# Performance work log

Measured on AMD Instinct MI355X. Metric: run time of the kernel, lower is better.

Reference implementation:

```python
import jax, jax.numpy as jnp
import numpy as np

P = 512        # n_predicates
C = 65536      # n_constants
L = 1          # max_rule_length (only runnable config of original code)


def setup_inputs() -> dict:
    key = jax.random.key(0)
    k1, k2 = jax.random.split(key)
    initial_facts = jax.random.uniform(k1, (P, C), dtype=jnp.float32)
    rule_weights = jax.random.normal(k2, (P, L, P), dtype=jnp.float32)
    return {"initial_facts": initial_facts, "rule_weights": rule_weights, "n_iterations": 3}


def reference(initial_facts, rule_weights, n_iterations):
    # F.softmax(rule[step], dim=0) on the 1-D vector rule_weights[r, 0, :]
    # == softmax over the last axis of rule_weights[:, 0, :].
    # Stacking apply_rule over all rules r is exactly A @ facts.
    A = jax.nn.softmax(rule_weights[:, 0, :], axis=-1)  # [P, P]
    facts = initial_facts                                # [P, C]
    for _ in range(n_iterations):
        derived = A @ facts                              # [P, C] (rule r -> row r)
        facts = jnp.maximum(facts, derived.max(axis=0))  # broadcast [C] over [P, C]
    return facts
```

## Files before the change

### kernel.cpp

```cpp
#include <hip/hip_runtime.h>
#include <hip/hip_bf16.h>
#include <cstdint>


typedef __attribute__((ext_vector_type(8))) short bf16x8;
typedef __attribute__((ext_vector_type(8))) unsigned short u16x8;
typedef __attribute__((ext_vector_type(4))) float f32x4;
typedef unsigned short ushort_t;
typedef unsigned int uint32;

#define PDIM 512
#define CDIM 65536
#define NT   64

__device__ __forceinline__ ushort_t f2bf(float x) {
    uint32 u = __float_as_uint(x);
    return (ushort_t)((u + 0x7fffu + ((u >> 16) & 1u)) >> 16);
}
__device__ __forceinline__ float bf2f(uint32 bits) { return __uint_as_float(bits << 16); }

__device__ __forceinline__ bf16x8 pkmax8(bf16x8 v, ushort_t mu) {
    u16x8 a = __builtin_bit_cast(u16x8, v);
    const u16x8 mb = {mu, mu, mu, mu, mu, mu, mu, mu};
    a = __builtin_elementwise_max(a, mb);
    return __builtin_bit_cast(bf16x8, a);
}

__global__ __launch_bounds__(64) void softmax_pack(const float* __restrict__ rw,
                                                   ushort_t* __restrict__ Apk) {
    const int r  = blockIdx.x;
    const int ln = threadIdx.x;
    const float* row = rw + r * PDIM;
    float4 x0 = *(const float4*)(row + ln * 8);
    float4 x1 = *(const float4*)(row + ln * 8 + 4);
    float v[8] = {x0.x, x0.y, x0.z, x0.w, x1.x, x1.y, x1.z, x1.w};

    float mx = -1e30f;
    #pragma unroll
    for (int i = 0; i < 8; ++i) mx = fmaxf(mx, v[i]);
    #pragma unroll
    for (int d = 1; d < 64; d <<= 1) mx = fmaxf(mx, __shfl_xor(mx, d, 64));
    float s = 0.f;
    #pragma unroll
    for (int i = 0; i < 8; ++i) { v[i] = __expf(v[i] - mx); s += v[i]; }
    #pragma unroll
    for (int d = 1; d < 64; d <<= 1) s += __shfl_xor(s, d, 64);
    const float inv = 1.f / s;

    ushort_t o[8];
    #pragma unroll
    for (int i = 0; i < 8; ++i) o[i] = f2bf(v[i] * inv);
    const int idx16 = (ln >> 2) * 2048 + (r >> 4) * 64 + ((ln & 3) << 4) + (r & 15);
    *(int4*)(Apk + idx16 * 8) = *(const int4*)o;
}

__global__ __launch_bounds__(256, 2) void ilp_kernel(
        const float* __restrict__ facts,
        const ushort_t* __restrict__ Apk,
        const int* __restrict__ n_iter_p,
        float* __restrict__ out) {
    __shared__ ushort_t ft[NT * PDIM];
    __shared__ float wred[2][4][NT];
    __shared__ float mfin[NT];

    const int tid  = threadIdx.x;
    const int wave = tid >> 6;
    const int lane = tid & 63;
    const int l15  = lane & 15;
    const int quad = lane >> 4;
    const int c0   = blockIdx.x * NT;

    {
        const int ch = (tid & 31) * 2;
        const int pb = tid >> 5;
        #pragma unroll 4
        for (int s = 0; s < 8; ++s) {
            const int p0 = s * 64 + pb * 8;
            ushort_t ga[8], gb[8];
            #pragma unroll
            for (int i = 0; i < 8; ++i) {
                const float2 v = *(const float2*)(facts + (p0 + i) * CDIM + c0 + ch);
                ga[i] = f2bf(v.x);
                gb[i] = f2bf(v.y);
            }
            const int g = p0 >> 3;
            *(int4*)(&ft[ch * PDIM + ((g ^ (ch & 7)) << 3)])             = *(const int4*)ga;
            *(int4*)(&ft[(ch + 1) * PDIM + ((g ^ ((ch + 1) & 7)) << 3)]) = *(const int4*)gb;
        }
    }
    __syncthreads();

    int n_iter = *n_iter_p;
    n_iter = n_iter < 0 ? 0 : (n_iter > 8 ? 8 : n_iter);

    const int abase = wave * 4096 + lane * 8;
    int cbase[4], cx8[4];
    #pragma unroll
    for (int ct = 0; ct < 4; ++ct) {
        const int c = ct * 16 + l15;
        cbase[ct] = c * PDIM;
        cx8[ct]   = (c & 7) * 8;
    }

    ushort_t ml[4] = {0, 0, 0, 0};
    float    mf[4] = {0.f, 0.f, 0.f, 0.f};

    bf16x8 aF[2][8], bF[2][4];
    {
        const ushort_t* ap = Apk + abase;
        #pragma unroll
        for (int rt = 0; rt < 8; ++rt) aF[0][rt] = *(const bf16x8*)(ap + rt * 512);
    }

    #pragma unroll 1
    for (int it = 0; it < n_iter; ++it) {
        f32x4 acc[8][4];
        #pragma unroll
        for (int rt = 0; rt < 8; ++rt)
            #pragma unroll
            for (int ct = 0; ct < 4; ++ct) acc[rt][ct] = (f32x4){0.f, 0.f, 0.f, 0.f};

        {
            const int g8 = quad * 8;
            #pragma unroll
            for (int ct = 0; ct < 4; ++ct)
                bF[0][ct] = pkmax8(*(const bf16x8*)(&ft[cbase[ct] + (g8 ^ cx8[ct])]), ml[ct]);
        }

        #pragma unroll 2
        for (int kt = 0; kt < 16; ++kt) {
            const int cur = kt & 1, nxt = cur ^ 1;
            const int ktn = (kt + 1) & 15;
            {
                const ushort_t* ap = Apk + abase + ktn * 16384;
                #pragma unroll
                for (int rt = 0; rt < 8; ++rt) aF[nxt][rt] = *(const bf16x8*)(ap + rt * 512);
            }
            {
                const int g8 = (ktn * 4 + quad) * 8;
                #pragma unroll
                for (int ct = 0; ct < 4; ++ct)
                    bF[nxt][ct] = pkmax8(*(const bf16x8*)(&ft[cbase[ct] + (g8 ^ cx8[ct])]), ml[ct]);
            }
            __builtin_amdgcn_s_setprio(1);
            #pragma unroll
            for (int rt = 0; rt < 8; ++rt)
                #pragma unroll
                for (int ct = 0; ct < 4; ++ct)
                    acc[rt][ct] = __builtin_amdgcn_mfma_f32_16x16x32_bf16(
                        aF[cur][rt], bF[cur][ct], acc[rt][ct], 0, 0, 0);
            __builtin_amdgcn_s_setprio(0);
        }

        float mx[4];
        #pragma unroll
        for (int ct = 0; ct < 4; ++ct) {
            float m0 = -1e30f;
            #pragma unroll
            for (int rt = 0; rt < 8; ++rt)
                #pragma unroll
                for (int e = 0; e < 4; ++e) m0 = fmaxf(m0, acc[rt][ct][e]);
            m0 = fmaxf(m0, __shfl_xor(m0, 16, 64));
            m0 = fmaxf(m0, __shfl_xor(m0, 32, 64));
            mx[ct] = m0;
        }
        const int buf = it & 1;
        if (quad == 0) {
            #pragma unroll
            for (int ct = 0; ct < 4; ++ct) wred[buf][wave][ct * 16 + l15] = mx[ct];
        }
        __syncthreads();
        #pragma unroll
        for (int ct = 0; ct < 4; ++ct) {
            const int c = ct * 16 + l15;
            const float m = fmaxf(fmaxf(wred[buf][0][c], wred[buf][1][c]),
                                  fmaxf(wred[buf][2][c], wred[buf][3][c]));
            mf[ct] = fmaxf(mf[ct], m);
            ml[ct] = f2bf(mf[ct]);
        }
    }

    if (wave == 0 && quad == 0) {
        #pragma unroll
        for (int ct = 0; ct < 4; ++ct) mfin[ct * 16 + l15] = mf[ct];
    }
    __syncthreads();

    {
        const int ch = (tid & 31) * 2;
        const int pb = tid >> 5;
        const float ma = mfin[ch];
        const float mb = mfin[ch + 1];
        for (int s = 0; s < 8; ++s) {
            const int p0 = s * 64 + pb * 8;
            const int g = p0 >> 3;
            ushort_t ga[8], gb[8];
            *(int4*)ga = *(const int4*)(&ft[ch * PDIM + ((g ^ (ch & 7)) << 3)]);
            *(int4*)gb = *(const int4*)(&ft[(ch + 1) * PDIM + ((g ^ ((ch + 1) & 7)) << 3)]);
            #pragma unroll
            for (int i = 0; i < 8; ++i) {
                float2 v;
                v.x = fmaxf(bf2f(ga[i]), ma);
                v.y = fmaxf(bf2f(gb[i]), mb);
                *(float2*)(out + (p0 + i) * CDIM + c0 + ch) = v;
            }
        }
    }
}

extern "C" void kernel_launch(void* const* d_in, const int* in_sizes, int n_in,
                              void* d_out, int out_size, void* d_ws, size_t ws_size,
                              hipStream_t stream) {
    const float* facts    = (const float*)d_in[0];
    const float* rw       = (const float*)d_in[1];
    const int*   n_iter_p = (const int*)d_in[2];
    float* out = (float*)d_out;

    ushort_t* Apk = (ushort_t*)d_ws;

    softmax_pack<<<PDIM, 64, 0, stream>>>(rw, Apk);
    ilp_kernel<<<CDIM / NT, 256, 0, stream>>>(facts, Apk, n_iter_p, out);
}
```

Measured before the change: 302.6 us.

## Switch matmul to 32x32x16 bf16 MFMA with repacked A and new LDS swizzle

Replaces the 16x16x32 MFMA tiling with 32x32x16 MFMA tiles. The softmax pack kernel's A layout and the LDS swizzle key for the facts tile are changed to match the new operand layout. The pkmax of the B operand is now applied after the prefetch rather than at load time, and the column-max reduction needs one fewer cross-lane shuffle. The aim is fewer MFMA issues and operand loads per K step. The larger per-instruction latency changes how the loop pipelines, and the LDS bank-conflict behaviour of the new swizzle is not certain.

```diff
diff --git a/kernel.cpp b/kernel.cpp
--- a/kernel.cpp
+++ b/kernel.cpp
@@ -5,7 +5,7 @@
 
 typedef __attribute__((ext_vector_type(8))) short bf16x8;
 typedef __attribute__((ext_vector_type(8))) unsigned short u16x8;
-typedef __attribute__((ext_vector_type(4))) float f32x4;
+typedef __attribute__((ext_vector_type(16))) float f32x16;
 typedef unsigned short ushort_t;
 typedef unsigned int uint32;
 
@@ -50,7 +50,7 @@
     ushort_t o[8];
     #pragma unroll
     for (int i = 0; i < 8; ++i) o[i] = f2bf(v[i] * inv);
-    const int idx16 = (ln >> 2) * 2048 + (r >> 4) * 64 + ((ln & 3) << 4) + (r & 15);
+    const int idx16 = ((ln >> 1) * 16 + (r >> 5)) * 64 + ((ln & 1) << 5) + (r & 31);
     *(int4*)(Apk + idx16 * 8) = *(const int4*)o;
 }
 
@@ -66,13 +66,17 @@
     const int tid  = threadIdx.x;
     const int wave = tid >> 6;
     const int lane = tid & 63;
-    const int l15  = lane & 15;
-    const int quad = lane >> 4;
+    const int l31  = lane & 31;
+    const int half = lane >> 5;
     const int c0   = blockIdx.x * NT;
 
+    int n_iter = *n_iter_p;
+    n_iter = n_iter < 0 ? 0 : (n_iter > 8 ? 8 : n_iter);
+
     {
-        const int ch = (tid & 31) * 2;
-        const int pb = tid >> 5;
+        const int ch  = (tid & 31) * 2;
+        const int pb  = tid >> 5;
+        const int key = ((ch >> 1) & 7) << 3;
         #pragma unroll 4
         for (int s = 0; s < 8; ++s) {
             const int p0 = s * 64 + pb * 8;
@@ -83,120 +87,118 @@
                 ga[i] = f2bf(v.x);
                 gb[i] = f2bf(v.y);
             }
-            const int g = p0 >> 3;
-            *(int4*)(&ft[ch * PDIM + ((g ^ (ch & 7)) << 3)])             = *(const int4*)ga;
-            *(int4*)(&ft[(ch + 1) * PDIM + ((g ^ ((ch + 1) & 7)) << 3)]) = *(const int4*)gb;
+            *(int4*)(&ft[ch * PDIM + (p0 ^ key)])       = *(const int4*)ga;
+            *(int4*)(&ft[(ch + 1) * PDIM + (p0 ^ key)]) = *(const int4*)gb;
         }
     }
     __syncthreads();
 
-    int n_iter = *n_iter_p;
-    n_iter = n_iter < 0 ? 0 : (n_iter > 8 ? 8 : n_iter);
-
-    const int abase = wave * 4096 + lane * 8;
-    int cbase[4], cx8[4];
-    #pragma unroll
-    for (int ct = 0; ct < 4; ++ct) {
-        const int c = ct * 16 + l15;
-        cbase[ct] = c * PDIM;
-        cx8[ct]   = (c & 7) * 8;
-    }
-
-    ushort_t ml[4] = {0, 0, 0, 0};
-    float    mf[4] = {0.f, 0.f, 0.f, 0.f};
-
-    bf16x8 aF[2][8], bF[2][4];
+    const ushort_t* abase = Apk + (wave * 256 + half * 32 + l31) * 8;
+    int cbase2[2], ckey2[2];
+    #pragma unroll
+    for (int ct2 = 0; ct2 < 2; ++ct2) {
+        const int c = ct2 * 32 + l31;
+        cbase2[ct2] = c * PDIM;
+        ckey2[ct2]  = ((c >> 1) & 7) << 3;
+    }
+
+    ushort_t ml[2] = {0, 0};
+    float    mf[2] = {0.f, 0.f};
+
+    bf16x8 aF[2][4], bR[2][2];
     {
-        const ushort_t* ap = Apk + abase;
-        #pragma unroll
-        for (int rt = 0; rt < 8; ++rt) aF[0][rt] = *(const bf16x8*)(ap + rt * 512);
+        #pragma unroll
+        for (int rt2 = 0; rt2 < 4; ++rt2) aF[0][rt2] = *(const bf16x8*)(abase + rt2 * 512);
+        const int gh = half * 8;
+        #pragma unroll
+        for (int ct2 = 0; ct2 < 2; ++ct2)
+            bR[0][ct2] = *(const bf16x8*)(&ft[cbase2[ct2] + (gh ^ ckey2[ct2])]);
     }
 
     #pragma unroll 1
     for (int it = 0; it < n_iter; ++it) {
-        f32x4 acc[8][4];
-        #pragma unroll
-        for (int rt = 0; rt < 8; ++rt)
-            #pragma unroll
-            for (int ct = 0; ct < 4; ++ct) acc[rt][ct] = (f32x4){0.f, 0.f, 0.f, 0.f};
-
-        {
-            const int g8 = quad * 8;
-            #pragma unroll
-            for (int ct = 0; ct < 4; ++ct)
-                bF[0][ct] = pkmax8(*(const bf16x8*)(&ft[cbase[ct] + (g8 ^ cx8[ct])]), ml[ct]);
-        }
+        f32x16 acc[4][2];
+        #pragma unroll
+        for (int rt2 = 0; rt2 < 4; ++rt2)
+            #pragma unroll
+            for (int ct2 = 0; ct2 < 2; ++ct2)
+                #pragma unroll
+                for (int e = 0; e < 16; ++e) acc[rt2][ct2][e] = 0.f;
 
         #pragma unroll 2
-        for (int kt = 0; kt < 16; ++kt) {
-            const int cur = kt & 1, nxt = cur ^ 1;
-            const int ktn = (kt + 1) & 15;
+        for (int kt2 = 0; kt2 < 32; ++kt2) {
+            const int cur = kt2 & 1, nxt = cur ^ 1;
+            const int ktn = (kt2 + 1) & 31;
             {
-                const ushort_t* ap = Apk + abase + ktn * 16384;
-                #pragma unroll
-                for (int rt = 0; rt < 8; ++rt) aF[nxt][rt] = *(const bf16x8*)(ap + rt * 512);
+                const ushort_t* ap = abase + ktn * 8192;
+                #pragma unroll
+                for (int rt2 = 0; rt2 < 4; ++rt2)
+                    aF[nxt][rt2] = *(const bf16x8*)(ap + rt2 * 512);
             }
             {
-                const int g8 = (ktn * 4 + quad) * 8;
-                #pragma unroll
-                for (int ct = 0; ct < 4; ++ct)
-                    bF[nxt][ct] = pkmax8(*(const bf16x8*)(&ft[cbase[ct] + (g8 ^ cx8[ct])]), ml[ct]);
-            }
+                const int gh = (ktn * 2 + half) * 8;
+                #pragma unroll
+                for (int ct2 = 0; ct2 < 2; ++ct2)
+                    bR[nxt][ct2] = *(const bf16x8*)(&ft[cbase2[ct2] + (gh ^ ckey2[ct2])]);
+            }
+            bf16x8 bC[2];
+            #pragma unroll
+            for (int ct2 = 0; ct2 < 2; ++ct2) bC[ct2] = pkmax8(bR[cur][ct2], ml[ct2]);
+
             __builtin_amdgcn_s_setprio(1);
             #pragma unroll
-            for (int rt = 0; rt < 8; ++rt)
-                #pragma unroll
-                for (int ct = 0; ct < 4; ++ct)
-                    acc[rt][ct] = __builtin_amdgcn_mfma_f32_16x16x32_bf16(
-                        aF[cur][rt], bF[cur][ct], acc[rt][ct], 0, 0, 0);
+            for (int rt2 = 0; rt2 < 4; ++rt2)
+                #pragma unroll
+                for (int ct2 = 0; ct2 < 2; ++ct2)
+                    acc[rt2][ct2] = __builtin_amdgcn_mfma_f32_32x32x16_bf16(
+                        aF[cur][rt2], bC[ct2], acc[rt2][ct2], 0, 0, 0);
             __builtin_amdgcn_s_setprio(0);
         }
 
-        float mx[4];
-        #pragma unroll
-        for (int ct = 0; ct < 4; ++ct) {
+        float mx[2];
+        #pragma unroll
+        for (int ct2 = 0; ct2 < 2; ++ct2) {
             float m0 = -1e30f;
             #pragma unroll
-            for (int rt = 0; rt < 8; ++rt)
-                #pragma unroll
-                for (int e = 0; e < 4; ++e) m0 = fmaxf(m0, acc[rt][ct][e]);
-            m0 = fmaxf(m0, __shfl_xor(m0, 16, 64));
+            for (int rt2 = 0; rt2 < 4; ++rt2)
+                #pragma unroll
+                for (int e = 0; e < 16; ++e) m0 = fmaxf(m0, acc[rt2][ct2][e]);
             m0 = fmaxf(m0, __shfl_xor(m0, 32, 64));
-            mx[ct] = m0;
+            mx[ct2] = m0;
         }
         const int buf = it & 1;
-        if (quad == 0) {
-            #pragma unroll
-            for (int ct = 0; ct < 4; ++ct) wred[buf][wave][ct * 16 + l15] = mx[ct];
+        if (half == 0) {
+            #pragma unroll
+            for (int ct2 = 0; ct2 < 2; ++ct2) wred[buf][wave][ct2 * 32 + l31] = mx[ct2];
         }
         __syncthreads();
         #pragma unroll
-        for (int ct = 0; ct < 4; ++ct) {
-            const int c = ct * 16 + l15;
+        for (int ct2 = 0; ct2 < 2; ++ct2) {
+            const int c = ct2 * 32 + l31;
             const float m = fmaxf(fmaxf(wred[buf][0][c], wred[buf][1][c]),
                                   fmaxf(wred[buf][2][c], wred[buf][3][c]));
-            mf[ct] = fmaxf(mf[ct], m);
-            ml[ct] = f2bf(mf[ct]);
-        }
-    }
-
-    if (wave == 0 && quad == 0) {
-        #pragma unroll
-        for (int ct = 0; ct < 4; ++ct) mfin[ct * 16 + l15] = mf[ct];
+            mf[ct2] = fmaxf(mf[ct2], m);
+            ml[ct2] = f2bf(mf[ct2]);
+        }
+    }
+
+    if (wave == 0 && half == 0) {
+        #pragma unroll
+        for (int ct2 = 0; ct2 < 2; ++ct2) mfin[ct2 * 32 + l31] = mf[ct2];
     }
     __syncthreads();
 
     {
-        const int ch = (tid & 31) * 2;
-        const int pb = tid >> 5;
+        const int ch  = (tid & 31) * 2;
+        const int pb  = tid >> 5;
+        const int key = ((ch >> 1) & 7) << 3;
         const float ma = mfin[ch];
         const float mb = mfin[ch + 1];
         for (int s = 0; s < 8; ++s) {
             const int p0 = s * 64 + pb * 8;
-            const int g = p0 >> 3;
             ushort_t ga[8], gb[8];
-            *(int4*)ga = *(const int4*)(&ft[ch * PDIM + ((g ^ (ch & 7)) << 3)]);
-            *(int4*)gb = *(const int4*)(&ft[(ch + 1) * PDIM + ((g ^ ((ch + 1) & 7)) << 3)]);
+            *(int4*)ga = *(const int4*)(&ft[ch * PDIM + (p0 ^ key)]);
+            *(int4*)gb = *(const int4*)(&ft[(ch + 1) * PDIM + (p0 ^ key)]);
             #pragma unroll
             for (int i = 0; i < 8; ++i) {
                 float2 v;
```

New measurement: 303.0 us. Within noise of the previous version (+0.1%).
